# Kernel optimization log

Hardware: AMD Instinct MI355X
Metric: run time of the kernel (lower is better)

Reference implementation:

```python
import jax, jax.numpy as jnp
import numpy as np

EPS = 1e-8  # torch F.cosine_similarity default eps
NEG = -1e9  # masked_fill value


def setup_inputs() -> dict:
    key = jax.random.key(0)
    k1, k2, k3 = jax.random.split(key, 3)
    B, Sq, Sk, D = 4, 2048, 2048, 1024
    query = jax.random.normal(k1, (B, Sq, 1, D), dtype=jnp.float32)
    key_t = jax.random.normal(k2, (B, 1, Sk, D), dtype=jnp.float32)
    mask = jax.random.randint(k3, (B, Sk), 0, 2, dtype=jnp.int32)
    return {"query": query, "key": key_t, "mask": mask}


def reference(query, key, mask):
    # query: [B, Sq, 1, D], key: [B, 1, Sk, D]
    q = query[:, :, 0, :]  # [B, Sq, D]
    k = key[:, 0, :, :]    # [B, Sk, D]
    # cosine_similarity(q, k, dim=3) = (q.k) / (max(|q|,eps) * max(|k|,eps))
    qn = jnp.maximum(jnp.linalg.norm(q, axis=-1), EPS)  # [B, Sq]
    kn = jnp.maximum(jnp.linalg.norm(k, axis=-1), EPS)  # [B, Sk]
    dot = jnp.einsum('bqd,bkd->bqk', q, k)              # [B, Sq, Sk]
    scores = dot / (qn[:, :, None] * kn[:, None, :])
    # mask.unsqueeze(1).repeat(1, Sq, 1) -> broadcast [B, 1, Sk] over Sq
    scores = jnp.where(mask[:, None, :] == 0, NEG, scores)
    return scores
```

## Files before the change

kernel.cpp:

```cpp
#include <hip/hip_runtime.h>
#include <hip/hip_bf16.h>
#include <stdint.h>


constexpr int B_  = 4;
constexpr int SQ  = 2048;
constexpr int SK  = 2048;
constexpr int D_  = 1024;
constexpr int BM  = 128;
constexpr int BN  = 128;
constexpr int BK  = 32;
constexpr int LDK = 48;

typedef __attribute__((ext_vector_type(8))) short   short8;
typedef __attribute__((ext_vector_type(4))) float   f32x4;
typedef __attribute__((ext_vector_type(4))) unsigned uint4v;

__device__ inline unsigned pack_bf16(float lo, float hi) {
  union { float f; unsigned u; } a, b;
  a.f = lo; b.f = hi;
  return __builtin_amdgcn_perm(b.u, a.u, 0x07060302u);
}

__global__ __launch_bounds__(256, 2) void ca_gemm(
    const float* __restrict__ Q,
    const float* __restrict__ Km,
    const int*   __restrict__ mask,
    float*       __restrict__ out)
{
  __shared__ __align__(16) short As[BM * LDK];
  __shared__ __align__(16) short Bs[BN * LDK];
  __shared__ float ssA_part[256];
  __shared__ float ssB_part[256];
  __shared__ float invA[BM];
  __shared__ float invB[BN];

  const int tid  = threadIdx.x;
  const int lane = tid & 63;
  const int w    = tid >> 6;
  const int b    = blockIdx.z;
  const int tm0  = blockIdx.y * BM;
  const int tn0  = blockIdx.x * BN;

  const int ra = tid >> 1;
  const int ka = (tid & 1) * 16;

  const float* qp = Q  + ((size_t)b * SQ + tm0 + ra) * D_ + ka;
  const float* kp = Km + ((size_t)b * SK + tn0 + ra) * D_ + ka;

  f32x4 zero4 = {0.0f, 0.0f, 0.0f, 0.0f};
  f32x4 acc[4][4];
  #pragma unroll
  for (int i = 0; i < 4; ++i)
    #pragma unroll
    for (int j = 0; j < 4; ++j) acc[i][j] = zero4;

  float ssA = 0.0f, ssB = 0.0f;

  const int wm = (w >> 1) * 64;
  const int wn = (w & 1) * 64;
  const int lr = lane & 15;
  const int lq = lane >> 4;

  short* aw = &As[ra * LDK + ka];
  short* bw = &Bs[ra * LDK + ka];

  for (int k0 = 0; k0 < D_; k0 += BK) {
    f32x4 av[4], bv[4];
    #pragma unroll
    for (int i = 0; i < 4; ++i) av[i] = *(const f32x4*)(qp + 4 * i);
    #pragma unroll
    for (int i = 0; i < 4; ++i) bv[i] = *(const f32x4*)(kp + 4 * i);
    qp += BK; kp += BK;

    unsigned pa[8], pb[8];
    #pragma unroll
    for (int i = 0; i < 4; ++i) {
      pa[2*i]   = pack_bf16(av[i].x, av[i].y);
      pa[2*i+1] = pack_bf16(av[i].z, av[i].w);
      pb[2*i]   = pack_bf16(bv[i].x, bv[i].y);
      pb[2*i+1] = pack_bf16(bv[i].z, bv[i].w);
      ssA += av[i].x*av[i].x + av[i].y*av[i].y + av[i].z*av[i].z + av[i].w*av[i].w;
      ssB += bv[i].x*bv[i].x + bv[i].y*bv[i].y + bv[i].z*bv[i].z + bv[i].w*bv[i].w;
    }

    __syncthreads();
    {
      uint4v wa0 = {pa[0], pa[1], pa[2], pa[3]};
      uint4v wa1 = {pa[4], pa[5], pa[6], pa[7]};
      uint4v wb0 = {pb[0], pb[1], pb[2], pb[3]};
      uint4v wb1 = {pb[4], pb[5], pb[6], pb[7]};
      *(uint4v*)(aw)     = wa0;
      *(uint4v*)(aw + 8) = wa1;
      *(uint4v*)(bw)     = wb0;
      *(uint4v*)(bw + 8) = wb1;
    }
    __syncthreads();

    short8 af[4], bf[4];
    #pragma unroll
    for (int t = 0; t < 4; ++t)
      af[t] = *(const short8*)&As[(wm + t * 16 + lr) * LDK + lq * 8];
    #pragma unroll
    for (int t = 0; t < 4; ++t)
      bf[t] = *(const short8*)&Bs[(wn + t * 16 + lr) * LDK + lq * 8];

    #pragma unroll
    for (int i = 0; i < 4; ++i)
      #pragma unroll
      for (int j = 0; j < 4; ++j)
        acc[i][j] = __builtin_amdgcn_mfma_f32_16x16x32_bf16(af[i], bf[j], acc[i][j], 0, 0, 0);
  }

  ssA_part[tid] = ssA;
  ssB_part[tid] = ssB;
  __syncthreads();
  if (tid < BM) {
    float s = ssA_part[2 * tid] + ssA_part[2 * tid + 1];
    invA[tid] = 1.0f / fmaxf(sqrtf(s), 1e-8f);
  } else {
    int r = tid - BM;
    float s = ssB_part[2 * r] + ssB_part[2 * r + 1];
    invB[r] = 1.0f / fmaxf(sqrtf(s), 1e-8f);
  }
  __syncthreads();

  #pragma unroll
  for (int tn = 0; tn < 4; ++tn) {
    const int lc = wn + tn * 16 + lr;
    const int gc = tn0 + lc;
    const int mk = mask[b * SK + gc];
    const float ib = invB[lc];
    #pragma unroll
    for (int tm = 0; tm < 4; ++tm) {
      const int lrow = wm + tm * 16 + lq * 4;
      #pragma unroll
      for (int r = 0; r < 4; ++r) {
        float v = mk ? acc[tm][tn][r] * invA[lrow + r] * ib : -1000000000.0f;
        out[((size_t)b * SQ + tm0 + lrow + r) * SK + gc] = v;
      }
    }
  }
}

extern "C" void kernel_launch(void* const* d_in, const int* in_sizes, int n_in,
                              void* d_out, int out_size, void* d_ws, size_t ws_size,
                              hipStream_t stream) {
  const float* Q    = (const float*)d_in[0];
  const float* Km   = (const float*)d_in[1];
  const int*   mask = (const int*)d_in[2];
  float*       out  = (float*)d_out;

  dim3 grid(SK / BN, SQ / BM, B_);
  ca_gemm<<<grid, dim3(256), 0, stream>>>(Q, Km, mask, out);
}
```

Before: 193.6 us.

## Pre-convert inputs to bf16 with norms, then GEMM via async global-to-LDS loads

After: 167.2 us. -13.7%, faster.

```diff
diff --git a/kernel.cpp b/kernel.cpp
--- a/kernel.cpp
+++ b/kernel.cpp
@@ -10,11 +10,11 @@
 constexpr int BM  = 128;
 constexpr int BN  = 128;
 constexpr int BK  = 32;
-constexpr int LDK = 48;
-
-typedef __attribute__((ext_vector_type(8))) short   short8;
-typedef __attribute__((ext_vector_type(4))) float   f32x4;
+
+typedef __attribute__((ext_vector_type(8))) short    short8;
+typedef __attribute__((ext_vector_type(4))) float    f32x4;
 typedef __attribute__((ext_vector_type(4))) unsigned uint4v;
+typedef unsigned int u32;
 
 __device__ inline unsigned pack_bf16(float lo, float hi) {
   union { float f; unsigned u; } a, b;
@@ -22,11 +22,146 @@
   return __builtin_amdgcn_perm(b.u, a.u, 0x07060302u);
 }
 
-__global__ __launch_bounds__(256, 2) void ca_gemm(
-    const float* __restrict__ Q,
-    const float* __restrict__ Km,
+__device__ inline void async_ld16(const void* g, void* l) {
+  __builtin_amdgcn_global_load_lds((const __attribute__((address_space(1))) u32*)g,
+                                   (__attribute__((address_space(3))) u32*)l, 16, 0, 0);
+}
+
+constexpr int ROWS_Q = B_ * SQ;
+constexpr int ROWS_T = B_ * (SQ + SK);
+
+__global__ __launch_bounds__(256) void convert_norm(
+    const float* __restrict__ Q, const float* __restrict__ Km,
+    unsigned short* __restrict__ Qb, unsigned short* __restrict__ Kb,
+    float* __restrict__ invQ, float* __restrict__ invK)
+{
+  const int row  = blockIdx.x * 4 + (threadIdx.x >> 6);
+  const int lane = threadIdx.x & 63;
+
+  const float* src; unsigned short* dst; float* inv;
+  if (row < ROWS_Q) {
+    src = Q  + (size_t)row * D_;
+    dst = Qb + (size_t)row * D_;
+    inv = invQ + row;
+  } else {
+    int r = row - ROWS_Q;
+    src = Km + (size_t)r * D_;
+    dst = Kb + (size_t)r * D_;
+    inv = invK + r;
+  }
+
+  const f32x4* s4 = (const f32x4*)(src + lane * 16);
+  f32x4 v[4];
+  #pragma unroll
+  for (int i = 0; i < 4; ++i) v[i] = s4[i];
+
+  float ss = 0.0f;
+  unsigned p[8];
+  #pragma unroll
+  for (int i = 0; i < 4; ++i) {
+    p[2*i]   = pack_bf16(v[i].x, v[i].y);
+    p[2*i+1] = pack_bf16(v[i].z, v[i].w);
+    ss += v[i].x*v[i].x + v[i].y*v[i].y + v[i].z*v[i].z + v[i].w*v[i].w;
+  }
+  uint4v w0 = {p[0], p[1], p[2], p[3]};
+  uint4v w1 = {p[4], p[5], p[6], p[7]};
+  uint4v* d4 = (uint4v*)(dst + lane * 16);
+  d4[0] = w0; d4[1] = w1;
+
+  #pragma unroll
+  for (int off = 32; off > 0; off >>= 1) ss += __shfl_xor(ss, off);
+  if (lane == 0) *inv = 1.0f / fmaxf(sqrtf(ss), 1e-8f);
+}
+
+__global__ __launch_bounds__(256, 2) void ca_gemm_bf(
+    const unsigned short* __restrict__ Qb,
+    const unsigned short* __restrict__ Kb,
+    const float* __restrict__ invQ,
+    const float* __restrict__ invK,
     const int*   __restrict__ mask,
     float*       __restrict__ out)
+{
+  __shared__ __align__(16) unsigned short As[BM * BK];
+  __shared__ __align__(16) unsigned short Bs[BN * BK];
+
+  const int tid  = threadIdx.x;
+  const int lane = tid & 63;
+  const int w    = tid >> 6;
+  const int b    = blockIdx.z;
+  const int tm0  = blockIdx.y * BM;
+  const int tn0  = blockIdx.x * BN;
+
+  const int srow = lane >> 2;
+  const int soff = (lane & 3) * 16;
+
+  const char* qrow = (const char*)(Qb + ((size_t)b * SQ + tm0 + w * 32 + srow) * D_) + soff;
+  const char* krow = (const char*)(Kb + ((size_t)b * SK + tn0 + w * 32 + srow) * D_) + soff;
+  const size_t rstep16 = (size_t)16 * D_ * 2;
+
+  unsigned short* ldsA0 = &As[(w * 32 +  0) * BK];
+  unsigned short* ldsA1 = &As[(w * 32 + 16) * BK];
+  unsigned short* ldsB0 = &Bs[(w * 32 +  0) * BK];
+  unsigned short* ldsB1 = &Bs[(w * 32 + 16) * BK];
+
+  f32x4 zero4 = {0.0f, 0.0f, 0.0f, 0.0f};
+  f32x4 acc[4][4];
+  #pragma unroll
+  for (int i = 0; i < 4; ++i)
+    #pragma unroll
+    for (int j = 0; j < 4; ++j) acc[i][j] = zero4;
+
+  const int wm = (w >> 1) * 64;
+  const int wn = (w & 1) * 64;
+  const int lr = lane & 15;
+  const int lq = lane >> 4;
+
+  for (int k0 = 0; k0 < D_; k0 += BK) {
+    __syncthreads();
+    const size_t kb = (size_t)k0 * 2;
+    async_ld16(qrow + kb,           ldsA0);
+    async_ld16(qrow + kb + rstep16, ldsA1);
+    async_ld16(krow + kb,           ldsB0);
+    async_ld16(krow + kb + rstep16, ldsB1);
+    __syncthreads();
+
+    short8 af[4], bf[4];
+    #pragma unroll
+    for (int t = 0; t < 4; ++t)
+      af[t] = *(const short8*)&As[(wm + t * 16 + lr) * BK + lq * 8];
+    #pragma unroll
+    for (int t = 0; t < 4; ++t)
+      bf[t] = *(const short8*)&Bs[(wn + t * 16 + lr) * BK + lq * 8];
+
+    #pragma unroll
+    for (int i = 0; i < 4; ++i)
+      #pragma unroll
+      for (int j = 0; j < 4; ++j)
+        acc[i][j] = __builtin_amdgcn_mfma_f32_16x16x32_bf16(af[i], bf[j], acc[i][j], 0, 0, 0);
+  }
+
+  #pragma unroll
+  for (int tn = 0; tn < 4; ++tn) {
+    const int gc = tn0 + wn + tn * 16 + lr;
+    const int mk = mask[b * SK + gc];
+    const float ib = invK[b * SK + gc];
+    #pragma unroll
+    for (int tm = 0; tm < 4; ++tm) {
+      const int lrow = wm + tm * 16 + lq * 4;
+      #pragma unroll
+      for (int r = 0; r < 4; ++r) {
+        const float ia = invQ[b * SQ + tm0 + lrow + r];
+        float v = mk ? acc[tm][tn][r] * ia * ib : -1000000000.0f;
+        out[((size_t)b * SQ + tm0 + lrow + r) * SK + gc] = v;
+      }
+    }
+  }
+}
+
+constexpr int LDK = 40;
+
+__global__ __launch_bounds__(256, 2) void ca_gemm(
+    const float* __restrict__ Q, const float* __restrict__ Km,
+    const int* __restrict__ mask, float* __restrict__ out)
 {
   __shared__ __align__(16) short As[BM * LDK];
   __shared__ __align__(16) short Bs[BN * LDK];
@@ -151,6 +286,20 @@
   const int*   mask = (const int*)d_in[2];
   float*       out  = (float*)d_out;
 
-  dim3 grid(SK / BN, SQ / BM, B_);
-  ca_gemm<<<grid, dim3(256), 0, stream>>>(Q, Km, mask, out);
-}
+  const size_t nQ   = (size_t)B_ * SQ * D_;
+  const size_t nK   = (size_t)B_ * SK * D_;
+  const size_t need = (nQ + nK) * 2
+                    + (size_t)B_ * (SQ + SK) * 4;
+  if (ws_size >= need) {
+    unsigned short* Qb  = (unsigned short*)d_ws;
+    unsigned short* Kb  = Qb + nQ;
+    float*          iQ  = (float*)(Kb + nK);
+    float*          iK  = iQ + (size_t)B_ * SQ;
+    convert_norm<<<ROWS_T / 4, 256, 0, stream>>>(Q, Km, Qb, Kb, iQ, iK);
+    dim3 grid(SK / BN, SQ / BM, B_);
+    ca_gemm_bf<<<grid, dim3(256), 0, stream>>>(Qb, Kb, iQ, iK, mask, out);
+  } else {
+    dim3 grid(SK / BN, SQ / BM, B_);
+    ca_gemm<<<grid, dim3(256), 0, stream>>>(Q, Km, mask, out);
+  }
+}
```
